# Kernel optimization log

Measured on AMD Instinct MI355X. Metric: run time of the kernel, lower is better.

Reference implementation:

```python
import jax, jax.numpy as jnp
import numpy as np

B, S, C = 4, 2048, 1024
DK = C // 4   # 256, q/k projection dim
DO = 1024     # out_channels


def setup_inputs() -> dict:
    key = jax.random.key(0)
    ks = jax.random.split(key, 7)
    s = 1.0 / np.sqrt(C)
    return {
        "x": jax.random.normal(ks[0], (B, S, C), dtype=jnp.float32),
        "Wq": jax.random.uniform(ks[1], (C, DK), jnp.float32, -s, s),
        "bq": jax.random.uniform(ks[2], (DK,), jnp.float32, -s, s),
        "Wk": jax.random.uniform(ks[3], (C, DK), jnp.float32, -s, s),
        "bk": jax.random.uniform(ks[4], (DK,), jnp.float32, -s, s),
        "Wv": jax.random.uniform(ks[5], (C, DO), jnp.float32, -s, s),
        "bv": jax.random.uniform(ks[6], (DO,), jnp.float32, -s, s),
    }


def reference(x, Wq, bq, Wk, bk, Wv, bv):
    q = jnp.einsum("bsc,cd->bsd", x, Wq) + bq   # [B,S,DK]
    k = jnp.einsum("bsc,cd->bsd", x, Wk) + bk   # [B,S,DK]
    v = jnp.einsum("bsc,cd->bsd", x, Wv) + bv   # [B,S,DO]
    scores = jnp.einsum("bqd,bkd->bqk", q, k) / jnp.sqrt(jnp.float32(DK))
    attn = jax.nn.softmax(scores, axis=-1)      # [B,S,S]
    return jnp.einsum("bqk,bkd->bqd", attn, v)  # [B,S,DO]
```

## Files before the change

### kernel.cpp

```cpp
#include <hip/hip_runtime.h>
#include <hip/hip_bf16.h>

typedef __attribute__((ext_vector_type(8))) short short8;
typedef __attribute__((ext_vector_type(8))) __bf16 bf16x8;
typedef __attribute__((ext_vector_type(4))) float f32x4;

#define MFMA(a, b, c) __builtin_amdgcn_mfma_f32_16x16x32_bf16((a), (b), (c), 0, 0, 0)
#define SCALE 0.0625f

static __device__ __forceinline__ void gload16(const void* g, void* l) {
  __builtin_amdgcn_global_load_lds(
      (const __attribute__((address_space(1))) void*)g,
      (__attribute__((address_space(3))) void*)l, 16, 0, 0);
}

static __device__ __forceinline__ unsigned short f2b(float f) {
  union { __hip_bfloat16 h; unsigned short u; } cv;
  cv.h = __float2bfloat16(f);
  return cv.u;
}

__global__ __launch_bounds__(256) void convert_x_kern(const float* __restrict__ x,
                                                      unsigned short* __restrict__ xb) {
  long i = ((long)blockIdx.x * 256 + threadIdx.x) * 8;
  float4 a = *reinterpret_cast<const float4*>(x + i);
  float4 b = *reinterpret_cast<const float4*>(x + i + 4);
  short8 o;
  o[0] = (short)f2b(a.x); o[1] = (short)f2b(a.y); o[2] = (short)f2b(a.z); o[3] = (short)f2b(a.w);
  o[4] = (short)f2b(b.x); o[5] = (short)f2b(b.y); o[6] = (short)f2b(b.z); o[7] = (short)f2b(b.w);
  *reinterpret_cast<short8*>(xb + i) = o;
}

__global__ void pack_bias_kern(const float* __restrict__ bq, const float* __restrict__ bk,
                               const float* __restrict__ bv, float* __restrict__ bc) {
  int i = blockIdx.x * 256 + threadIdx.x;
  float v = (i < 256) ? bq[i] : (i < 512) ? bk[i - 256] : bv[i - 512];
  bc[i] = v;
}

__global__ __launch_bounds__(256) void transpose_w_kern(const float* __restrict__ src,
                                                        unsigned short* __restrict__ dst,
                                                        int ldsrc, int lddst) {
  __shared__ __align__(16) unsigned short tile[64][72];
  int r0 = blockIdx.y * 64, c0 = blockIdx.x * 64;
  int t = threadIdx.x;
  #pragma unroll
  for (int it = 0; it < 4; ++it) {
    int idx = it * 1024 + t * 4;
    int row = idx >> 6, col = idx & 63;
    float4 v = *reinterpret_cast<const float4*>(src + (long)(r0 + row) * ldsrc + c0 + col);
    tile[row][col + 0] = f2b(v.x); tile[row][col + 1] = f2b(v.y);
    tile[row][col + 2] = f2b(v.z); tile[row][col + 3] = f2b(v.w);
  }
  __syncthreads();
  #pragma unroll
  for (int it = 0; it < 4; ++it) {
    int idx = it * 1024 + t * 4;
    int orow = idx >> 6, ocol = idx & 63;
    ushort4 o;
    o.x = tile[ocol + 0][orow]; o.y = tile[ocol + 1][orow];
    o.z = tile[ocol + 2][orow]; o.w = tile[ocol + 3][orow];
    *reinterpret_cast<ushort4*>(dst + (long)(c0 + orow) * lddst + r0 + ocol) = o;
  }
}

__global__ __launch_bounds__(256) void transpose_v_kern(const unsigned short* __restrict__ src0,
                                                        unsigned short* __restrict__ dst0,
                                                        int ldsrc, int lddst,
                                                        long sbatch, long dbatch) {
  const unsigned short* src = src0 + (long)blockIdx.z * sbatch;
  unsigned short* dst = dst0 + (long)blockIdx.z * dbatch;
  __shared__ __align__(16) unsigned short tile[64][72];
  int r0 = blockIdx.y * 64, c0 = blockIdx.x * 64;
  int t = threadIdx.x;
  #pragma unroll
  for (int it = 0; it < 2; ++it) {
    int idx = it * 2048 + t * 8;
    int row = idx >> 6, col = idx & 63;
    short8 v = *reinterpret_cast<const short8*>(src + (long)(r0 + row) * ldsrc + c0 + col);
    *reinterpret_cast<short8*>(&tile[row][col]) = v;
  }
  __syncthreads();
  #pragma unroll
  for (int it = 0; it < 2; ++it) {
    int idx = it * 2048 + t * 8;
    int orow = idx >> 6, ocol = idx & 63;
    short8 o;
    #pragma unroll
    for (int i = 0; i < 8; ++i) o[i] = (short)tile[ocol + i][orow];
    *reinterpret_cast<short8*>(dst + (long)(c0 + orow) * lddst + r0 + ocol) = o;
  }
}

template <int BM, int SWZ, bool BF16OUT, bool BIAS, bool RS, bool EXPSUM>
__global__ __launch_bounds__(512, 2) void gemm_pi(
    const unsigned short* __restrict__ A, const unsigned short* __restrict__ B,
    const float* __restrict__ bias, void* __restrict__ Cout,
    int NT, int lda, int ldb, int ldc,
    long batchA, long batchB, long batchC,
    const float* __restrict__ rowscale,
    float* __restrict__ lpart) {
  constexpr int WM = BM / 2;
  constexpr int MH = WM / 64;
  constexpr int ASH = BM * 64;
  constexpr int TSH = ASH + 256 * 64;
  constexpr int NBUF = (BM == 256) ? 2 : 3;
  __shared__ __align__(128) unsigned short lds[NBUF * TSH];

  int bid = blockIdx.x;
  int b = 0, tm, tn;
  if constexpr (SWZ == 0) {
    int xcd = bid & 7, s = bid >> 3;
    tm = xcd * 4 + s / 6; tn = s % 6;
  } else if constexpr (SWZ == 1) {
    int xcd = bid & 7, s = bid >> 3;
    b = xcd >> 1; tm = (xcd & 1) * 4 + (s >> 3); tn = s & 7;
  } else {
    int xcd = bid & 7, s = bid >> 3;
    b = xcd >> 1; tm = (xcd & 1) * 8 + (s >> 2); tn = s & 3;
  }

  int t = threadIdx.x, w = t >> 6, l = t & 63;
  int wr = w >> 2, wc = w & 3;
  int g = l >> 4, c = l & 15;

  f32x4 acc[WM / 16][4];
  #pragma unroll
  for (int m = 0; m < WM / 16; ++m)
    #pragma unroll
    for (int n = 0; n < 4; ++n) acc[m][n] = (f32x4){0.f, 0.f, 0.f, 0.f};

  int srow = t >> 3;
  int scb = (t & 7) * 16;

  const unsigned short* aptr = A + (long)b * batchA + (long)(tm * BM) * lda;
  const unsigned short* bptr = B + (long)b * batchB + (long)(tn * 256) * ldb;

  int kb = scb ^ ((srow & 7) << 4);

  auto stageA = [&](int buf, int k0, int r) {
    int row = r * 64 + srow;
    gload16(aptr + (long)row * lda + k0 + (kb >> 1),
            lds + buf * TSH + r * 4096 + t * 8);
  };
  auto stageB = [&](int buf, int k0, int r) {
    int row = r * 64 + srow;
    gload16(bptr + (long)row * ldb + k0 + (kb >> 1),
            lds + buf * TSH + ASH + r * 4096 + t * 8);
  };

  auto ldA = [&](const char* abase, int mh, int kh, int m) {
    int row = wr * WM + mh * 64 + m * 16 + c;
    int pb = row * 128 + (kh * 32 + g * 8) * 2;
    pb ^= ((pb >> 7) & 7) << 4;
    return *reinterpret_cast<const bf16x8*>(abase + pb);
  };
  auto ldB = [&](const char* bbase, int kh, int n) {
    int row = wc * 64 + n * 16 + c;
    int pb = row * 128 + (kh * 32 + g * 8) * 2;
    pb ^= ((pb >> 7) & 7) << 4;
    return *reinterpret_cast<const bf16x8*>(bbase + pb);
  };

  if constexpr (BM == 256) {
    stageB(0, 0, 0); stageB(0, 0, 1); stageB(0, 0, 2); stageB(0, 0, 3);
    stageA(0, 0, 0); stageA(0, 0, 2); stageA(0, 0, 1); stageA(0, 0, 3);
    asm volatile("s_waitcnt vmcnt(0)" ::: "memory");
    __builtin_amdgcn_s_barrier();

    for (int kt = 0; kt < NT; ++kt) {
      int cur = kt & 1, nb = cur ^ 1;
      const char* abase = (const char*)(lds + cur * TSH);
      const char* bbase = (const char*)(lds + cur * TSH + ASH);
      bool more = (kt + 1) < NT;
      int k1 = (kt + 1) * 64;
      bf16x8 bfr[4];
      #pragma unroll
      for (int p = 0; p < 4; ++p) {
        const int kh = p >> 1, mh = p & 1;
        bf16x8 af[4];
        #pragma unroll
        for (int m = 0; m < 4; ++m) af[m] = ldA(abase, mh, kh, m);
        if (mh == 0) {
          #pragma unroll
          for (int n = 0; n < 4; ++n) bfr[n] = ldB(bbase, kh, n);
        }
        if (more) {
          if      (p == 0) { stageB(nb, k1, 0); stageB(nb, k1, 1); }
          else if (p == 1) { stageB(nb, k1, 2); stageB(nb, k1, 3); }
          else if (p == 2) { stageA(nb, k1, 0); stageA(nb, k1, 2); }
          else             { stageA(nb, k1, 1); stageA(nb, k1, 3); }
        }
        __builtin_amdgcn_s_barrier();
        asm volatile("s_waitcnt lgkmcnt(0)" ::: "memory");
        __builtin_amdgcn_sched_barrier(0);
        __builtin_amdgcn_s_setprio(1);
        #pragma unroll
        for (int m = 0; m < 4; ++m)
          #pragma unroll
          for (int n = 0; n < 4; ++n)
            acc[mh * 4 + m][n] = MFMA(af[m], bfr[n], acc[mh * 4 + m][n]);
        __builtin_amdgcn_s_setprio(0);
        if (p == 0) {
          if (kt == NT - 1) asm volatile("s_waitcnt vmcnt(0)" ::: "memory");
          else              asm volatile("s_waitcnt vmcnt(2)" ::: "memory");
        }
        if (p == 3 && more) {
          asm volatile("s_waitcnt vmcnt(2)" ::: "memory");
        }
        __builtin_amdgcn_s_barrier();
      }
    }
  } else {
    auto stage6 = [&](int buf, int kt2, int ph) {
      int k0 = kt2 * 64;
      if (ph == 0) { stageB(buf, k0, 0); stageB(buf, k0, 1); stageB(buf, k0, 2); }
      else         { stageB(buf, k0, 3); stageA(buf, k0, 0); stageA(buf, k0, 1); }
    };
    stage6(0, 0, 0); stage6(0, 0, 1);
    stage6(1, 1, 0); stage6(1, 1, 1);
    asm volatile("s_waitcnt vmcnt(6)" ::: "memory");
    __builtin_amdgcn_s_barrier();

    for (int kt = 0; kt < NT; ++kt) {
      int cur = kt % 3, nb = (kt + 2) % 3;
      const char* abase = (const char*)(lds + cur * TSH);
      const char* bbase = (const char*)(lds + cur * TSH + ASH);
      bool more2 = (kt + 2) < NT;
      #pragma unroll
      for (int p = 0; p < 2; ++p) {
        const int kh = p;
        bf16x8 af[4], bfr[4];
        #pragma unroll
        for (int m = 0; m < 4; ++m) af[m] = ldA(abase, 0, kh, m);
        #pragma unroll
        for (int n = 0; n < 4; ++n) bfr[n] = ldB(bbase, kh, n);
        if (more2) stage6(nb, kt + 2, p);
        __builtin_amdgcn_s_barrier();
        asm volatile("s_waitcnt lgkmcnt(0)" ::: "memory");
        __builtin_amdgcn_sched_barrier(0);
        __builtin_amdgcn_s_setprio(1);
        #pragma unroll
        for (int m = 0; m < 4; ++m)
          #pragma unroll
          for (int n = 0; n < 4; ++n)
            acc[m][n] = MFMA(af[m], bfr[n], acc[m][n]);
        __builtin_amdgcn_s_setprio(0);
        if (p == 1) {
          if (kt < NT - 2)       asm volatile("s_waitcnt vmcnt(6)" ::: "memory");
          else if (kt == NT - 2) asm volatile("s_waitcnt vmcnt(0)" ::: "memory");
        }
        __builtin_amdgcn_s_barrier();
      }
    }
  }

  int rbase = tm * BM + wr * WM + g * 4;
  int c0 = tn * 256 + wc * 64 + c;

  if constexpr (EXPSUM) {
    __shared__ float lred[4][BM];
    #pragma unroll
    for (int mi = 0; mi < WM / 16; ++mi) {
      int roff = (mi / 4) * 64 + (mi % 4) * 16;
      #pragma unroll
      for (int j = 0; j < 4; ++j) {
        long ob = (long)b * batchC + (long)(rbase + roff + j) * ldc + c0;
        float rs = 0.f;
        #pragma unroll
        for (int n = 0; n < 4; ++n) {
          float pv = __expf(acc[mi][n][j] * SCALE);
          ((unsigned short*)Cout)[ob + n * 16] = f2b(pv);
          rs += pv;
        }
        rs += __shfl_xor(rs, 1); rs += __shfl_xor(rs, 2);
        rs += __shfl_xor(rs, 4); rs += __shfl_xor(rs, 8);
        if (c == 0) lred[wc][wr * WM + roff + g * 4 + j] = rs;
      }
    }
    __syncthreads();
    for (int rr = t; rr < BM; rr += 512) {
      float s = lred[0][rr] + lred[1][rr] + lred[2][rr] + lred[3][rr];
      lpart[((long)b * 2048 + tm * BM + rr) * 8 + tn] = s;
    }
  } else {
    #pragma unroll
    for (int mi = 0; mi < WM / 16; ++mi) {
      int roff = (mi / 4) * 64 + (mi % 4) * 16;
      float lv[4];
      if (RS) {
        #pragma unroll
        for (int j = 0; j < 4; ++j)
          lv[j] = rowscale[(long)b * 2048 + rbase + roff + j];
      }
      #pragma unroll
      for (int n = 0; n < 4; ++n) {
        int col = c0 + n * 16;
        float bv = BIAS ? bias[col] : 0.f;
        long rowb = (long)b * batchC + (long)(rbase + roff) * ldc + col;
        #pragma unroll
        for (int j = 0; j < 4; ++j) {
          float v = acc[mi][n][j] + bv;
          if (RS) v *= lv[j];
          if (BF16OUT) ((unsigned short*)Cout)[rowb + (long)j * ldc] = f2b(v);
          else         ((float*)Cout)[rowb + (long)j * ldc] = v;
        }
      }
    }
  }
}

__global__ __launch_bounds__(256) void linv_kern(const float* __restrict__ lpart,
                                                 float* __restrict__ linv) {
  int r = blockIdx.x * 256 + threadIdx.x;
  float s = 0.f;
  #pragma unroll
  for (int i = 0; i < 8; ++i) s += lpart[(long)r * 8 + i];
  linv[r] = 1.f / s;
}

extern "C" void kernel_launch(void* const* d_in, const int* in_sizes, int n_in,
                              void* d_out, int out_size, void* d_ws, size_t ws_size,
                              hipStream_t stream) {
  (void)in_sizes; (void)n_in; (void)out_size; (void)ws_size;
  const float* x  = (const float*)d_in[0];
  const float* Wq = (const float*)d_in[1];
  const float* bq = (const float*)d_in[2];
  const float* Wk = (const float*)d_in[3];
  const float* bk = (const float*)d_in[4];
  const float* Wv = (const float*)d_in[5];
  const float* bv = (const float*)d_in[6];
  float* out = (float*)d_out;
  char* ws = (char*)d_ws;

  unsigned short* xb   = (unsigned short*)(ws + 0);
  float*          lpart= (float*)         (ws + 0);
  float*          linv = (float*)         (ws + 262144);
  unsigned short* wt   = (unsigned short*)(ws + 16777216);
  float*          bc   = (float*)         (ws + 19922944);
  unsigned short* qkv  = (unsigned short*)(ws + 19929088);
  unsigned short* vT   = (unsigned short*)(ws + 45094912);
  unsigned short* attn = (unsigned short*)(ws + 61872128);

  convert_x_kern<<<4096, 256, 0, stream>>>(x, xb);
  pack_bias_kern<<<6, 256, 0, stream>>>(bq, bk, bv, bc);
  transpose_w_kern<<<dim3(4, 16), 256, 0, stream>>>(Wq, wt,              256, 1024);
  transpose_w_kern<<<dim3(4, 16), 256, 0, stream>>>(Wk, wt + 256 * 1024, 256, 1024);
  transpose_w_kern<<<dim3(16, 16), 256, 0, stream>>>(Wv, wt + 512 * 1024, 1024, 1024);

  gemm_pi<256, 0, true, true, false, false><<<dim3(192), 512, 0, stream>>>(
      xb, wt, bc, qkv, 16, 1024, 1024, 1536, 0, 0, 0, nullptr, nullptr);

  transpose_v_kern<<<dim3(16, 32, 4), 256, 0, stream>>>(
      qkv + 512, vT, 1536, 2048, (long)2048 * 1536, (long)1024 * 2048);

  gemm_pi<256, 1, true, false, false, true><<<dim3(256), 512, 0, stream>>>(
      qkv, qkv + 256, nullptr, attn, 4, 1536, 1536, 2048,
      (long)2048 * 1536, (long)2048 * 1536, (long)2048 * 2048, nullptr, lpart);
  linv_kern<<<32, 256, 0, stream>>>(lpart, linv);

  gemm_pi<128, 2, false, false, true, false><<<dim3(256), 512, 0, stream>>>(
      attn, vT, nullptr, out, 32, 2048, 2048, 1024,
      (long)2048 * 2048, (long)1024 * 2048, (long)2048 * 1024, linv, nullptr);
}
```

Baseline: 123.7 us.

## Split attn·V GEMM into dedicated kernel with ping-pong warp-row staggering

```diff
diff --git a/kernel.cpp b/kernel.cpp
--- a/kernel.cpp
+++ b/kernel.cpp
@@ -101,23 +101,18 @@
     const float* __restrict__ rowscale,
     float* __restrict__ lpart) {
   constexpr int WM = BM / 2;
-  constexpr int MH = WM / 64;
   constexpr int ASH = BM * 64;
   constexpr int TSH = ASH + 256 * 64;
-  constexpr int NBUF = (BM == 256) ? 2 : 3;
-  __shared__ __align__(128) unsigned short lds[NBUF * TSH];
+  __shared__ __align__(128) unsigned short lds[2 * TSH];
 
   int bid = blockIdx.x;
   int b = 0, tm, tn;
   if constexpr (SWZ == 0) {
     int xcd = bid & 7, s = bid >> 3;
     tm = xcd * 4 + s / 6; tn = s % 6;
-  } else if constexpr (SWZ == 1) {
+  } else {
     int xcd = bid & 7, s = bid >> 3;
     b = xcd >> 1; tm = (xcd & 1) * 4 + (s >> 3); tn = s & 7;
-  } else {
-    int xcd = bid & 7, s = bid >> 3;
-    b = xcd >> 1; tm = (xcd & 1) * 8 + (s >> 2); tn = s & 3;
   }
 
   int t = threadIdx.x, w = t >> 6, l = t & 63;
@@ -132,10 +127,8 @@
 
   int srow = t >> 3;
   int scb = (t & 7) * 16;
-
   const unsigned short* aptr = A + (long)b * batchA + (long)(tm * BM) * lda;
   const unsigned short* bptr = B + (long)b * batchB + (long)(tn * 256) * ldb;
-
   int kb = scb ^ ((srow & 7) << 4);
 
   auto stageA = [&](int buf, int k0, int r) {
@@ -148,7 +141,6 @@
     gload16(bptr + (long)row * ldb + k0 + (kb >> 1),
             lds + buf * TSH + ASH + r * 4096 + t * 8);
   };
-
   auto ldA = [&](const char* abase, int mh, int kh, int m) {
     int row = wr * WM + mh * 64 + m * 16 + c;
     int pb = row * 128 + (kh * 32 + g * 8) * 2;
@@ -162,96 +154,52 @@
     return *reinterpret_cast<const bf16x8*>(bbase + pb);
   };
 
-  if constexpr (BM == 256) {
-    stageB(0, 0, 0); stageB(0, 0, 1); stageB(0, 0, 2); stageB(0, 0, 3);
-    stageA(0, 0, 0); stageA(0, 0, 2); stageA(0, 0, 1); stageA(0, 0, 3);
-    asm volatile("s_waitcnt vmcnt(0)" ::: "memory");
-    __builtin_amdgcn_s_barrier();
-
-    for (int kt = 0; kt < NT; ++kt) {
-      int cur = kt & 1, nb = cur ^ 1;
-      const char* abase = (const char*)(lds + cur * TSH);
-      const char* bbase = (const char*)(lds + cur * TSH + ASH);
-      bool more = (kt + 1) < NT;
-      int k1 = (kt + 1) * 64;
-      bf16x8 bfr[4];
-      #pragma unroll
-      for (int p = 0; p < 4; ++p) {
-        const int kh = p >> 1, mh = p & 1;
-        bf16x8 af[4];
-        #pragma unroll
-        for (int m = 0; m < 4; ++m) af[m] = ldA(abase, mh, kh, m);
-        if (mh == 0) {
-          #pragma unroll
-          for (int n = 0; n < 4; ++n) bfr[n] = ldB(bbase, kh, n);
-        }
-        if (more) {
-          if      (p == 0) { stageB(nb, k1, 0); stageB(nb, k1, 1); }
-          else if (p == 1) { stageB(nb, k1, 2); stageB(nb, k1, 3); }
-          else if (p == 2) { stageA(nb, k1, 0); stageA(nb, k1, 2); }
-          else             { stageA(nb, k1, 1); stageA(nb, k1, 3); }
-        }
-        __builtin_amdgcn_s_barrier();
-        asm volatile("s_waitcnt lgkmcnt(0)" ::: "memory");
-        __builtin_amdgcn_sched_barrier(0);
-        __builtin_amdgcn_s_setprio(1);
-        #pragma unroll
-        for (int m = 0; m < 4; ++m)
-          #pragma unroll
-          for (int n = 0; n < 4; ++n)
-            acc[mh * 4 + m][n] = MFMA(af[m], bfr[n], acc[mh * 4 + m][n]);
-        __builtin_amdgcn_s_setprio(0);
-        if (p == 0) {
-          if (kt == NT - 1) asm volatile("s_waitcnt vmcnt(0)" ::: "memory");
-          else              asm volatile("s_waitcnt vmcnt(2)" ::: "memory");
-        }
-        if (p == 3 && more) {
-          asm volatile("s_waitcnt vmcnt(2)" ::: "memory");
-        }
-        __builtin_amdgcn_s_barrier();
-      }
-    }
-  } else {
-    auto stage6 = [&](int buf, int kt2, int ph) {
-      int k0 = kt2 * 64;
-      if (ph == 0) { stageB(buf, k0, 0); stageB(buf, k0, 1); stageB(buf, k0, 2); }
-      else         { stageB(buf, k0, 3); stageA(buf, k0, 0); stageA(buf, k0, 1); }
-    };
-    stage6(0, 0, 0); stage6(0, 0, 1);
-    stage6(1, 1, 0); stage6(1, 1, 1);
-    asm volatile("s_waitcnt vmcnt(6)" ::: "memory");
-    __builtin_amdgcn_s_barrier();
-
-    for (int kt = 0; kt < NT; ++kt) {
-      int cur = kt % 3, nb = (kt + 2) % 3;
-      const char* abase = (const char*)(lds + cur * TSH);
-      const char* bbase = (const char*)(lds + cur * TSH + ASH);
-      bool more2 = (kt + 2) < NT;
-      #pragma unroll
-      for (int p = 0; p < 2; ++p) {
-        const int kh = p;
-        bf16x8 af[4], bfr[4];
-        #pragma unroll
-        for (int m = 0; m < 4; ++m) af[m] = ldA(abase, 0, kh, m);
+  stageB(0, 0, 0); stageB(0, 0, 1); stageB(0, 0, 2); stageB(0, 0, 3);
+  stageA(0, 0, 0); stageA(0, 0, 2); stageA(0, 0, 1); stageA(0, 0, 3);
+  asm volatile("s_waitcnt vmcnt(0)" ::: "memory");
+  __builtin_amdgcn_s_barrier();
+
+  for (int kt = 0; kt < NT; ++kt) {
+    int cur = kt & 1, nb = cur ^ 1;
+    const char* abase = (const char*)(lds + cur * TSH);
+    const char* bbase = (const char*)(lds + cur * TSH + ASH);
+    bool more = (kt + 1) < NT;
+    int k1 = (kt + 1) * 64;
+    bf16x8 bfr[4];
+    #pragma unroll
+    for (int p = 0; p < 4; ++p) {
+      const int kh = p >> 1, mh = p & 1;
+      bf16x8 af[4];
+      #pragma unroll
+      for (int m = 0; m < 4; ++m) af[m] = ldA(abase, mh, kh, m);
+      if (mh == 0) {
         #pragma unroll
         for (int n = 0; n < 4; ++n) bfr[n] = ldB(bbase, kh, n);
-        if (more2) stage6(nb, kt + 2, p);
-        __builtin_amdgcn_s_barrier();
-        asm volatile("s_waitcnt lgkmcnt(0)" ::: "memory");
-        __builtin_amdgcn_sched_barrier(0);
-        __builtin_amdgcn_s_setprio(1);
+      }
+      if (more) {
+        if      (p == 0) { stageB(nb, k1, 0); stageB(nb, k1, 1); }
+        else if (p == 1) { stageB(nb, k1, 2); stageB(nb, k1, 3); }
+        else if (p == 2) { stageA(nb, k1, 0); stageA(nb, k1, 2); }
+        else             { stageA(nb, k1, 1); stageA(nb, k1, 3); }
+      }
+      __builtin_amdgcn_s_barrier();
+      asm volatile("s_waitcnt lgkmcnt(0)" ::: "memory");
+      __builtin_amdgcn_sched_barrier(0);
+      __builtin_amdgcn_s_setprio(1);
+      #pragma unroll
+      for (int m = 0; m < 4; ++m)
         #pragma unroll
-        for (int m = 0; m < 4; ++m)
-          #pragma unroll
-          for (int n = 0; n < 4; ++n)
-            acc[m][n] = MFMA(af[m], bfr[n], acc[m][n]);
-        __builtin_amdgcn_s_setprio(0);
-        if (p == 1) {
-          if (kt < NT - 2)       asm volatile("s_waitcnt vmcnt(6)" ::: "memory");
-          else if (kt == NT - 2) asm volatile("s_waitcnt vmcnt(0)" ::: "memory");
-        }
-        __builtin_amdgcn_s_barrier();
-      }
+        for (int n = 0; n < 4; ++n)
+          acc[mh * 4 + m][n] = MFMA(af[m], bfr[n], acc[mh * 4 + m][n]);
+      __builtin_amdgcn_s_setprio(0);
+      if (p == 0) {
+        if (kt == NT - 1) asm volatile("s_waitcnt vmcnt(0)" ::: "memory");
+        else              asm volatile("s_waitcnt vmcnt(2)" ::: "memory");
+      }
+      if (p == 3 && more) {
+        asm volatile("s_waitcnt vmcnt(2)" ::: "memory");
+      }
+      __builtin_amdgcn_s_barrier();
     }
   }
 
@@ -306,6 +254,124 @@
           else         ((float*)Cout)[rowb + (long)j * ldc] = v;
         }
       }
+    }
+  }
+}
+
+__global__ __launch_bounds__(512, 2) void gemm_pp(
+    const unsigned short* __restrict__ A, const unsigned short* __restrict__ B,
+    float* __restrict__ Cout,
+    int NT, int lda, int ldb, int ldc,
+    long batchA, long batchB, long batchC,
+    const float* __restrict__ rowscale) {
+  constexpr int ASH = 128 * 64;
+  constexpr int TSH = ASH + 256 * 64;
+  __shared__ __align__(128) unsigned short lds[3 * TSH];
+
+  int bid = blockIdx.x;
+  int xcd = bid & 7, s = bid >> 3;
+  int b = xcd >> 1;
+  int tm = (xcd & 1) * 8 + (s >> 2), tn = s & 3;
+
+  int t = threadIdx.x, w = t >> 6, l = t & 63;
+  int wr = w >> 2, wc = w & 3;
+  int g = l >> 4, c = l & 15;
+
+  f32x4 acc[4][4];
+  #pragma unroll
+  for (int m = 0; m < 4; ++m)
+    #pragma unroll
+    for (int n = 0; n < 4; ++n) acc[m][n] = (f32x4){0.f, 0.f, 0.f, 0.f};
+
+  int srow = t >> 3;
+  int scb = (t & 7) * 16;
+  int kb = scb ^ ((srow & 7) << 4);
+  const unsigned short* aptr = A + (long)b * batchA + (long)(tm * 128) * lda;
+  const unsigned short* bptr = B + (long)b * batchB + (long)(tn * 256) * ldb;
+
+  auto stage6 = [&](int buf, int kt2) {
+    int k0 = kt2 * 64;
+    #pragma unroll
+    for (int r = 0; r < 4; ++r) {
+      int row = r * 64 + srow;
+      gload16(bptr + (long)row * ldb + k0 + (kb >> 1),
+              lds + buf * TSH + ASH + r * 4096 + t * 8);
+    }
+    #pragma unroll
+    for (int r = 0; r < 2; ++r) {
+      int row = r * 64 + srow;
+      gload16(aptr + (long)row * lda + k0 + (kb >> 1),
+              lds + buf * TSH + r * 4096 + t * 8);
+    }
+  };
+
+  stage6(0, 0); stage6(1, 1);
+  asm volatile("s_waitcnt vmcnt(6)" ::: "memory");
+  __builtin_amdgcn_s_barrier();
+  if (wr == 1) __builtin_amdgcn_s_barrier();
+
+  for (int hs = 0; hs < 2 * NT; ++hs) {
+    int kt = hs >> 1, kh = hs & 1;
+    const char* abase = (const char*)(lds + (kt % 3) * TSH);
+    const char* bbase = abase + ASH * 2;
+
+    bf16x8 af[4], bfr[4];
+    #pragma unroll
+    for (int m = 0; m < 4; ++m) {
+      int row = wr * 64 + m * 16 + c;
+      int pb = row * 128 + (kh * 32 + g * 8) * 2;
+      pb ^= ((pb >> 7) & 7) << 4;
+      af[m] = *reinterpret_cast<const bf16x8*>(abase + pb);
+    }
+    #pragma unroll
+    for (int n = 0; n < 4; ++n) {
+      int row = wc * 64 + n * 16 + c;
+      int pb = row * 128 + (kh * 32 + g * 8) * 2;
+      pb ^= ((pb >> 7) & 7) << 4;
+      bfr[n] = *reinterpret_cast<const bf16x8*>(bbase + pb);
+    }
+
+    if (kh == 1) {
+      if (kt + 2 < NT) stage6((kt + 2) % 3, kt + 2);
+      if (wr == 1) {
+        if (kt < NT - 2)       asm volatile("s_waitcnt vmcnt(6)" ::: "memory");
+        else if (kt == NT - 2) asm volatile("s_waitcnt vmcnt(0)" ::: "memory");
+      }
+    }
+    __builtin_amdgcn_s_barrier();
+    asm volatile("s_waitcnt lgkmcnt(0)" ::: "memory");
+    __builtin_amdgcn_sched_barrier(0);
+    __builtin_amdgcn_s_setprio(1);
+    #pragma unroll
+    for (int m = 0; m < 4; ++m)
+      #pragma unroll
+      for (int n = 0; n < 4; ++n)
+        acc[m][n] = MFMA(af[m], bfr[n], acc[m][n]);
+    __builtin_amdgcn_s_setprio(0);
+    if (kh == 1 && wr == 0) {
+      if (kt < NT - 2)       asm volatile("s_waitcnt vmcnt(6)" ::: "memory");
+      else if (kt == NT - 2) asm volatile("s_waitcnt vmcnt(0)" ::: "memory");
+    }
+    __builtin_amdgcn_s_barrier();
+  }
+  if (wr == 0) __builtin_amdgcn_s_barrier();
+
+  int rbase = tm * 128 + wr * 64 + g * 4;
+  int c0 = tn * 256 + wc * 64 + c;
+  #pragma unroll
+  for (int mi = 0; mi < 4; ++mi) {
+    int roff = mi * 16;
+    float lv[4];
+    #pragma unroll
+    for (int j = 0; j < 4; ++j)
+      lv[j] = rowscale[(long)b * 2048 + rbase + roff + j];
+    #pragma unroll
+    for (int n = 0; n < 4; ++n) {
+      int col = c0 + n * 16;
+      long rowb = (long)b * batchC + (long)(rbase + roff) * ldc + col;
+      #pragma unroll
+      for (int j = 0; j < 4; ++j)
+        Cout[rowb + (long)j * ldc] = acc[mi][n][j] * lv[j];
     }
   }
 }
@@ -359,7 +425,7 @@
       (long)2048 * 1536, (long)2048 * 1536, (long)2048 * 2048, nullptr, lpart);
   linv_kern<<<32, 256, 0, stream>>>(lpart, linv);
 
-  gemm_pi<128, 2, false, false, true, false><<<dim3(256), 512, 0, stream>>>(
-      attn, vT, nullptr, out, 32, 2048, 2048, 1024,
-      (long)2048 * 2048, (long)1024 * 2048, (long)2048 * 1024, linv, nullptr);
-}
+  gemm_pp<<<dim3(256), 512, 0, stream>>>(
+      attn, vT, out, 32, 2048, 2048, 1024,
+      (long)2048 * 2048, (long)1024 * 2048, (long)2048 * 1024, linv);
+}
```

Result: no change. 123.0 us (-0.6%).
